# Optimization experiments

Hardware: AMD Instinct MI355X
Metric: run time of the kernel (lower is better)

Reference implementation:

```python
import jax, jax.numpy as jnp
import numpy as np

# --- config (matches init_kwargs) ---
D_MODEL = 512
N_HEADS = 8
DIM_HEAD = D_MODEL // N_HEADS  # 64
BUCKET_SIZE = 64
N_HASHES = 4
B = 4
N = 4096
SELF_ATTN_VALUE = -5e4  # TOKEN_SELF_ATTN_VALUE in reformer_pytorch


def setup_inputs() -> dict:
    key = jax.random.key(0)
    ks = jax.random.split(key, 8)
    n_buckets = N // BUCKET_SIZE
    dh = N_HEADS * DIM_HEAD
    return {
        "queries": jax.random.normal(ks[0], (B, N, D_MODEL), jnp.float32),
        "keys": jax.random.normal(ks[1], (B, N, D_MODEL), jnp.float32),      # unused by module
        "values": jax.random.normal(ks[2], (B, N, D_MODEL), jnp.float32),    # unused by module
        "W_qk": jax.random.normal(ks[3], (D_MODEL, dh), jnp.float32) / np.float32(np.sqrt(D_MODEL)),
        "W_v": jax.random.normal(ks[4], (D_MODEL, dh), jnp.float32) / np.float32(np.sqrt(D_MODEL)),
        "W_out": jax.random.normal(ks[5], (dh, D_MODEL), jnp.float32) / np.float32(np.sqrt(dh)),
        "b_out": jnp.zeros((D_MODEL,), jnp.float32),
        # random LSH rotations: generated fresh (non-learnable) in torch; fixed here for determinism
        "rotations": jax.random.normal(ks[6], (DIM_HEAD, N_HASHES, n_buckets // 2), jnp.float32),
    }


def _look_one_back(x):
    # concat each chunk with the previous chunk along the within-chunk axis
    return jnp.concatenate([x, jnp.roll(x, 1, axis=1)], axis=2)


def lsh_attention(qk, v, rotations):
    # qk, v: (BH, T, dh) shared-QK LSH attention (reformer_pytorch LSHAttention)
    bh, T, dh = qk.shape
    n_buckets = T // BUCKET_SIZE
    total = N_HASHES * T

    # --- hash_vectors: random rotations + argmax over [R, -R] ---
    rotated = jnp.einsum('btf,fhi->bhti', qk, rotations)          # (bh, n_hashes, T, nb/2)
    rotated = jnp.concatenate([rotated, -rotated], axis=-1)       # (bh, n_hashes, T, nb)
    buckets = jnp.argmax(rotated, axis=-1)                        # (bh, n_hashes, T)
    offsets = (jnp.arange(N_HASHES) * n_buckets)[None, :, None]
    buckets = (buckets + offsets).reshape(bh, total)

    # --- stable sort by (bucket, position); keys are unique ---
    ticker = jnp.broadcast_to(jnp.arange(total)[None, :], (bh, total))
    buckets_and_t = T * buckets + (ticker % T)
    sticker = jnp.argsort(buckets_and_t, axis=-1)                 # (bh, total)
    undo_sort = jnp.argsort(sticker, axis=-1)
    st = sticker % T                                              # original positions, sorted

    sqk = jnp.take_along_axis(qk, st[:, :, None], axis=1)         # (bh, total, dh)
    sv = jnp.take_along_axis(v, st[:, :, None], axis=1)

    # --- chunk into bins; attend within chunk + one chunk back ---
    chunks = N_HASHES * n_buckets                                 # per-chunk len == BUCKET_SIZE
    bq_t = st.reshape(bh, chunks, -1)
    bqk = sqk.reshape(bh, chunks, -1, dh)
    bv = sv.reshape(bh, chunks, -1, dh)

    bq = bqk
    bk = bqk / jnp.maximum(jnp.linalg.norm(bqk, axis=-1, keepdims=True), 1e-12)  # F.normalize

    bk = _look_one_back(bk)       # (bh, chunks, 2*bs, dh)
    bv = _look_one_back(bv)
    bkv_t = _look_one_back(bq_t)  # (bh, chunks, 2*bs)

    dots = jnp.einsum('bcie,bcje->bcij', bq, bk) * (dh ** -0.5)   # (bh, chunks, bs, 2*bs)
    self_mask = bq_t[:, :, :, None] == bkv_t[:, :, None, :]
    dots = jnp.where(self_mask, SELF_ATTN_VALUE, dots)

    lse = jax.scipy.special.logsumexp(dots, axis=-1, keepdims=True)
    probs = jnp.exp(dots - lse)
    bo = jnp.einsum('bcij,bcje->bcie', probs, bv)                 # (bh, chunks, bs, dh)

    so = bo.reshape(bh, total, dh)
    slogits = lse.reshape(bh, total)
    o = jnp.take_along_axis(so, undo_sort[:, :, None], axis=1)
    logits = jnp.take_along_axis(slogits, undo_sort, axis=1)

    o = o.reshape(bh, N_HASHES, T, dh)
    logits = logits.reshape(bh, N_HASHES, T, 1)
    # combine hash rounds by softmax over per-round logsumexps
    w = jnp.exp(logits - jax.scipy.special.logsumexp(logits, axis=1, keepdims=True))
    return jnp.sum(o * w, axis=1)                                 # (bh, T, dh)


def reference(queries, keys, values, W_qk, W_v, W_out, b_out, rotations):
    Bsz, T, _ = queries.shape
    qk = queries @ W_qk                                           # (B, T, H*dh), no bias
    v = queries @ W_v

    def merge(x):
        return x.reshape(Bsz, T, N_HEADS, DIM_HEAD).transpose(0, 2, 1, 3).reshape(Bsz * N_HEADS, T, DIM_HEAD)

    out = lsh_attention(merge(qk), merge(v), rotations)           # (B*H, T, dh)
    out = out.reshape(Bsz, N_HEADS, T, DIM_HEAD).transpose(0, 2, 1, 3).reshape(Bsz, T, N_HEADS * DIM_HEAD)
    return out @ W_out + b_out                                    # to_out (with bias)
```

## Files before the change

### kernel.cpp

```cpp
#include <hip/hip_runtime.h>

typedef unsigned int uint32;
typedef _Float16 f16;
typedef _Float16 f16x8 __attribute__((ext_vector_type(8)));
typedef float f32x4 __attribute__((ext_vector_type(4)));
typedef unsigned short u16x8 __attribute__((ext_vector_type(8)));

#define B_SZ 4
#define T_SZ 4096
#define DMODEL 512
#define NHEAD 8
#define DH 64
#define NHASH 4
#define BH (B_SZ*NHEAD)
#define NBUCK 256
#define TOT (NHASH*T_SZ)
#define M_TOK (B_SZ*T_SZ)

#define KSTRIDE 72
#define PSTRIDE 136

#define AMB_TAU 1.5e-3f

__global__ __launch_bounds__(256) void kprep(
    const float* __restrict__ Wqk, const float* __restrict__ Wv,
    const float* __restrict__ Wout, f16* __restrict__ Wth, f16* __restrict__ Wtl,
    const float* __restrict__ rot, f16* __restrict__ rotTh, f16* __restrict__ rotTl,
    const float* __restrict__ qin, f16* __restrict__ Ah, f16* __restrict__ Al,
    int* __restrict__ amb_cnt)
{
  int bx = blockIdx.x;
  int tid = threadIdx.x;
  if (bx == 0 && tid == 0) *amb_cnt = 0;
  if (bx < 6){
    int n = bx*256 + tid;
    int sel = n >> 9, col = n & 511;
    const float* src = (sel==0)? Wqk : (sel==1)? Wv : Wout;
    f16* dh = Wth + (size_t)n*512;
    f16* dl = Wtl + (size_t)n*512;
    for (int kb=0; kb<64; kb++){
      f16x8 hv, lv;
      #pragma unroll
      for (int e=0;e<8;e++){
        float v = src[(size_t)(kb*8+e)*512 + col];
        f16 h = (f16)v;
        hv[e] = h; lv[e] = (f16)(v - (float)h);
      }
      ((f16x8*)dh)[kb] = hv;
      ((f16x8*)dl)[kb] = lv;
    }
  } else if (bx == 6){
    if (tid < 128){
      int n = tid;
      f16* dh = rotTh + n*64;
      f16* dl = rotTl + n*64;
      for (int db=0; db<8; db++){
        f16x8 hv, lv;
        #pragma unroll
        for (int e=0;e<8;e++){
          float v = rot[(db*8+e)*128 + n];
          f16 h = (f16)v;
          hv[e] = h; lv[e] = (f16)(v - (float)h);
        }
        ((f16x8*)dh)[db] = hv;
        ((f16x8*)dl)[db] = lv;
      }
    }
  } else {
    size_t gid = (size_t)(bx - 7)*256 + tid;
    const float4* src = (const float4*)(qin) + gid*2;
    float4 x0 = src[0], x1 = src[1];
    float v[8] = {x0.x,x0.y,x0.z,x0.w, x1.x,x1.y,x1.z,x1.w};
    f16x8 h, l;
    #pragma unroll
    for (int e=0;e<8;e++){ f16 hh=(f16)v[e]; h[e]=hh; l[e]=(f16)(v[e]-(float)hh); }
    ((f16x8*)Ah)[gid] = h;
    ((f16x8*)Al)[gid] = l;
  }
}

__global__ __launch_bounds__(256) void g_qkv(const f16* __restrict__ Ah,
    const f16* __restrict__ Al, const f16* __restrict__ Wth, const f16* __restrict__ Wtl,
    f16* __restrict__ qk16, f16* __restrict__ qkl, f16* __restrict__ v16)
{
  __shared__ f16 ah[128*KSTRIDE], al[128*KSTRIDE], bh[128*KSTRIDE], bl[128*KSTRIDE];
  int tid = threadIdx.x;
  int m0 = blockIdx.x*128, n0 = blockIdx.y*128;
  int w = tid >> 6, lane = tid & 63;
  int wm = w >> 1, wn = w & 1;
  int c_lane = lane & 15, quad = lane >> 4;

  f32x4 acc[4][4];
  #pragma unroll
  for (int mi=0;mi<4;mi++)
    #pragma unroll
    for (int ni=0;ni<4;ni++) acc[mi][ni] = (f32x4){0.f,0.f,0.f,0.f};

  int sr = tid >> 1, sc = (tid & 1) * 32;

  f16x8 pA[4], pAl[4], pB[4], pBl[4];
  auto issue = [&](int kc){
    int k0 = kc*64;
    const f16x8* pah = (const f16x8*)(Ah + (size_t)(m0+sr)*512 + k0 + sc);
    const f16x8* pal = (const f16x8*)(Al + (size_t)(m0+sr)*512 + k0 + sc);
    const f16x8* pbh = (const f16x8*)(Wth + (size_t)(n0+sr)*512 + k0 + sc);
    const f16x8* pbl = (const f16x8*)(Wtl + (size_t)(n0+sr)*512 + k0 + sc);
    #pragma unroll
    for (int i=0;i<4;i++){ pA[i]=pah[i]; pAl[i]=pal[i]; pB[i]=pbh[i]; pBl[i]=pbl[i]; }
  };

  issue(0);

  for (int kc=0; kc<8; kc++){
    {
      f16x8* dah = (f16x8*)&ah[sr*KSTRIDE + sc];
      f16x8* dal = (f16x8*)&al[sr*KSTRIDE + sc];
      f16x8* dbh = (f16x8*)&bh[sr*KSTRIDE + sc];
      f16x8* dbl = (f16x8*)&bl[sr*KSTRIDE + sc];
      #pragma unroll
      for (int i=0;i<4;i++){ dah[i]=pA[i]; dal[i]=pAl[i]; dbh[i]=pB[i]; dbl[i]=pBl[i]; }
    }
    __syncthreads();
    if (kc < 7) issue(kc+1);
    f16x8 fah[4][2], fal[4][2], fbh[4][2], fbl[4][2];
    #pragma unroll
    for (int i=0;i<4;i++)
      #pragma unroll
      for (int kb=0;kb<2;kb++){
        int ma = (wm*64 + i*16 + c_lane)*KSTRIDE + kb*32 + quad*8;
        int nb = (wn*64 + i*16 + c_lane)*KSTRIDE + kb*32 + quad*8;
        fah[i][kb] = *(const f16x8*)&ah[ma];
        fal[i][kb] = *(const f16x8*)&al[ma];
        fbh[i][kb] = *(const f16x8*)&bh[nb];
        fbl[i][kb] = *(const f16x8*)&bl[nb];
      }
    #pragma unroll
    for (int kb=0;kb<2;kb++)
      #pragma unroll
      for (int p=0;p<3;p++)
        #pragma unroll
        for (int mi=0;mi<4;mi++)
          #pragma unroll
          for (int ni=0;ni<4;ni++){
            f16x8 a = (p==2)? fal[mi][kb] : fah[mi][kb];
            f16x8 b = (p==1)? fbl[ni][kb] : fbh[ni][kb];
            acc[mi][ni] = __builtin_amdgcn_mfma_f32_16x16x32_f16(a, b, acc[mi][ni], 0,0,0);
          }
    __syncthreads();
  }

  #pragma unroll
  for (int mi=0;mi<4;mi++)
    #pragma unroll
    for (int ni=0;ni<4;ni++)
      #pragma unroll
      for (int r=0;r<4;r++){
        int n = n0 + wn*64 + ni*16 + c_lane;
        int tok = m0 + wm*64 + mi*16 + quad*4 + r;
        float val = acc[mi][ni][r];
        int b = tok >> 12, tp = tok & 4095;
        if (n < 512){
          int head = n >> 6, dd = n & 63;
          size_t idx = ((size_t)(b*NHEAD+head)*T_SZ + tp)*DH + dd;
          f16 hv = (f16)val;
          qk16[idx] = hv;
          qkl[idx]  = (f16)(val - (float)hv);
        } else {
          int j = n - 512, head = j >> 6, dd = j & 63;
          size_t idx = ((size_t)(b*NHEAD+head)*T_SZ + tp)*DH + dd;
          v16[idx] = (f16)val;
        }
      }
}

__global__ __launch_bounds__(256) void g_out(const float* __restrict__ lse,
    const f16* __restrict__ o_f16, const f16* __restrict__ Wth, const f16* __restrict__ Wtl,
    const float* __restrict__ bout, float* __restrict__ out)
{
  __shared__ f16 ah[128*KSTRIDE], al[128*KSTRIDE], bh[128*KSTRIDE], bl[128*KSTRIDE];
  int tid = threadIdx.x;
  int m0 = blockIdx.x*128, n0 = blockIdx.y*128;
  int w = tid >> 6, lane = tid & 63;
  int wm = w >> 1, wn = w & 1;
  int c_lane = lane & 15, quad = lane >> 4;
  const f16* Bh_base = Wth + (size_t)1024*512;
  const f16* Bl_base = Wtl + (size_t)1024*512;

  f32x4 acc[4][4];
  #pragma unroll
  for (int mi=0;mi<4;mi++)
    #pragma unroll
    for (int ni=0;ni<4;ni++) acc[mi][ni] = (f32x4){0.f,0.f,0.f,0.f};

  int sr = tid >> 1, sc = (tid & 1) * 32;
  int tok = m0 + sr;
  int tb = tok >> 12, tt = tok & 4095;

  float pl0, pl1, pl2, pl3;
  f16x8 pr0[4], pr1[4], pr2[4], pr3[4];

  auto issueA = [&](int kc){
    size_t lbase = ((size_t)(tb*NHEAD + kc)*NHASH)*T_SZ + tt;
    pl0 = lse[lbase];
    pl1 = lse[lbase + T_SZ];
    pl2 = lse[lbase + 2*T_SZ];
    pl3 = lse[lbase + 3*T_SZ];
    const f16x8* r0 = (const f16x8*)(o_f16 + lbase*DH + sc);
    const f16x8* r1 = (const f16x8*)(o_f16 + (lbase + (size_t)T_SZ)*DH + sc);
    const f16x8* r2 = (const f16x8*)(o_f16 + (lbase + (size_t)2*T_SZ)*DH + sc);
    const f16x8* r3 = (const f16x8*)(o_f16 + (lbase + (size_t)3*T_SZ)*DH + sc);
    #pragma unroll
    for (int i=0;i<4;i++){ pr0[i]=r0[i]; pr1[i]=r1[i]; pr2[i]=r2[i]; pr3[i]=r3[i]; }
  };

  issueA(0);

  for (int kc=0; kc<8; kc++){
    int k0 = kc*64;
    {
      float M = fmaxf(fmaxf(pl0,pl1), fmaxf(pl2,pl3));
      float e0 = __expf(pl0-M), e1 = __expf(pl1-M), e2 = __expf(pl2-M), e3 = __expf(pl3-M);
      float inv = 1.0f/(e0+e1+e2+e3);
      float w0=e0*inv, w1=e1*inv, w2=e2*inv, w3=e3*inv;
      const f16x8* pbhp = (const f16x8*)(Bh_base + (size_t)(n0+sr)*512 + k0 + sc);
      const f16x8* pblp = (const f16x8*)(Bl_base + (size_t)(n0+sr)*512 + k0 + sc);
      f16x8* dah = (f16x8*)&ah[sr*KSTRIDE + sc];
      f16x8* dal = (f16x8*)&al[sr*KSTRIDE + sc];
      f16x8* dbh = (f16x8*)&bh[sr*KSTRIDE + sc];
      f16x8* dbl = (f16x8*)&bl[sr*KSTRIDE + sc];
      #pragma unroll
      for (int i=0;i<4;i++){
        f16x8 a = pr0[i], bb = pr1[i], cc = pr2[i], dd = pr3[i];
        f16x8 ho, lo;
        #pragma unroll
        for (int e=0;e<8;e++){
          float res = w0*(float)a[e] + w1*(float)bb[e] + w2*(float)cc[e] + w3*(float)dd[e];
          f16 hh = (f16)res;
          ho[e] = hh; lo[e] = (f16)(res - (float)hh);
        }
        dah[i] = ho; dal[i] = lo;
        dbh[i] = pbhp[i]; dbl[i] = pblp[i];
      }
    }
    __syncthreads();
    if (kc < 7) issueA(kc+1);
    f16x8 fah[4][2], fal[4][2], fbh[4][2], fbl[4][2];
    #pragma unroll
    for (int i=0;i<4;i++)
      #pragma unroll
      for (int kb=0;kb<2;kb++){
        int ma = (wm*64 + i*16 + c_lane)*KSTRIDE + kb*32 + quad*8;
        int nb = (wn*64 + i*16 + c_lane)*KSTRIDE + kb*32 + quad*8;
        fah[i][kb] = *(const f16x8*)&ah[ma];
        fal[i][kb] = *(const f16x8*)&al[ma];
        fbh[i][kb] = *(const f16x8*)&bh[nb];
        fbl[i][kb] = *(const f16x8*)&bl[nb];
      }
    #pragma unroll
    for (int kb=0;kb<2;kb++)
      #pragma unroll
      for (int p=0;p<3;p++)
        #pragma unroll
        for (int mi=0;mi<4;mi++)
          #pragma unroll
          for (int ni=0;ni<4;ni++){
            f16x8 a = (p==2)? fal[mi][kb] : fah[mi][kb];
            f16x8 b = (p==1)? fbl[ni][kb] : fbh[ni][kb];
            acc[mi][ni] = __builtin_amdgcn_mfma_f32_16x16x32_f16(a, b, acc[mi][ni], 0,0,0);
          }
    __syncthreads();
  }

  #pragma unroll
  for (int mi=0;mi<4;mi++)
    #pragma unroll
    for (int ni=0;ni<4;ni++){
      int n = n0 + wn*64 + ni*16 + c_lane;
      float bn = bout[n];
      #pragma unroll
      for (int r=0;r<4;r++){
        int tk2 = m0 + wm*64 + mi*16 + quad*4 + r;
        out[(size_t)tk2*512 + n] = acc[mi][ni][r] + bn;
      }
    }
}

__global__ __launch_bounds__(256, 4) void k2_mfma(const f16* __restrict__ qkh,
    const f16* __restrict__ qkl, const f16* __restrict__ rotTh, const f16* __restrict__ rotTl,
    unsigned short* __restrict__ bucket,
    int* __restrict__ amb_list, int* __restrict__ amb_cnt)
{
  int tid = threadIdx.x;
  int w = tid >> 6, lane = tid & 63;
  int c_lane = lane & 15, quad = lane >> 4;
  int tok0 = (blockIdx.x*4 + w)*16;
  size_t rowb = (size_t)(tok0 + c_lane)*64;

  f16x8 tbh[2], tbl[2];
  #pragma unroll
  for (int kb=0;kb<2;kb++){
    tbh[kb] = *(const f16x8*)&qkh[rowb + kb*32 + quad*8];
    tbl[kb] = *(const f16x8*)&qkl[rowb + kb*32 + quad*8];
  }

  f32x4 acc[8];
  #pragma unroll
  for (int mi=0;mi<8;mi++) acc[mi] = (f32x4){0.f,0.f,0.f,0.f};

  #pragma unroll
  for (int mi=0;mi<8;mi++){
    int aoff = (mi*16 + c_lane)*64;
    #pragma unroll
    for (int kb=0;kb<2;kb++){
      f16x8 arh = *(const f16x8*)&rotTh[aoff + kb*32 + quad*8];
      f16x8 arl = *(const f16x8*)&rotTl[aoff + kb*32 + quad*8];
      acc[mi] = __builtin_amdgcn_mfma_f32_16x16x32_f16(arh, tbh[kb], acc[mi], 0,0,0);
      acc[mi] = __builtin_amdgcn_mfma_f32_16x16x32_f16(arl, tbh[kb], acc[mi], 0,0,0);
      acc[mi] = __builtin_amdgcn_mfma_f32_16x16x32_f16(arh, tbl[kb], acc[mi], 0,0,0);
    }
  }

  int tokg = tok0 + c_lane;
  int bhh = tokg >> 12, t = tokg & 4095;

  #pragma unroll
  for (int h=0; h<4; h++){
    float m1 = -1e30f, m2 = -1e30f, ssq = 0.f; int b1 = 0;
    #pragma unroll
    for (int u=0; u<8; u++){
      float v = acc[2*h + (u>>2)][u&3];
      int bidd = (u>>2)*16 + quad*4 + (u&3);
      ssq += v*v;
      if (v > m1){ m2=m1; m1=v; b1=bidd; } else if (v > m2) m2=v;
      float nv = -v;
      if (nv > m1){ m2=m1; m1=nv; b1=bidd+32; } else if (nv > m2) m2=nv;
    }
    #pragma unroll
    for (int d2=16; d2<64; d2<<=1){
      float om1 = __shfl_xor(m1, d2);
      float om2 = __shfl_xor(m2, d2);
      int   ob1 = __shfl_xor(b1, d2);
      ssq += __shfl_xor(ssq, d2);
      if (om1 > m1){ m2 = fmaxf(m1, om2); m1 = om1; b1 = ob1; }
      else          { m2 = fmaxf(m2, om1); }
    }
    if (quad == 0){
      float rms = sqrtf(ssq * (1.0f/32.0f));
      if (m1 - m2 < AMB_TAU * rms){
        int idx = atomicAdd(amb_cnt, 1);
        amb_list[idx] = (bhh<<14) | (h<<12) | t;
      } else {
        bucket[((bhh*NHASH + h)<<12) + t] = (unsigned short)(b1 + (h<<6));
      }
    }
  }
}

__global__ __launch_bounds__(256) void k2_fix(const float* __restrict__ qin,
    const float* __restrict__ Wqk, const float* __restrict__ rot,
    const int* __restrict__ amb_list, const int* __restrict__ amb_cnt,
    unsigned short* __restrict__ bucket)
{
  __shared__ __align__(16) float qs[512];
  __shared__ double part[4][64];
  __shared__ double qk64[64];
  __shared__ double accs[32];
  int n = *amb_cnt;
  int tid = threadIdx.x;
  int j = tid & 63, chunk = tid >> 6;
  for (int it = blockIdx.x; it < n; it += gridDim.x){
    int gid = amb_list[it];
    int t = gid & (T_SZ-1);
    int h = (gid >> 12) & 3;
    int bh = gid >> 14;
    int b = bh >> 3, head = bh & 7;
    if (tid < 128)
      *(float4*)&qs[tid*4] = ((const float4*)(qin + ((size_t)b*T_SZ + t)*DMODEL))[tid];
    __syncthreads();
    const float* wcol = Wqk + head*64 + j;
    int d0 = chunk*128;
    double s = 0.0;
    #pragma unroll 16
    for (int d=0; d<128; d++)
      s += (double)qs[d0+d] * (double)wcol[(size_t)(d0+d)*512];
    part[chunk][j] = s;
    __syncthreads();
    if (tid < 64)
      qk64[tid] = ((part[0][tid] + part[1][tid]) + part[2][tid]) + part[3][tid];
    __syncthreads();
    if (tid < 32){
      double a = 0.0;
      #pragma unroll 16
      for (int f=0; f<64; f++)
        a += qk64[f] * (double)rot[f*(NHASH*32) + h*32 + tid];
      accs[tid] = a;
    }
    __syncthreads();
    if (tid == 0){
      double best = accs[0]; int bk = 0;
      for (int k=1;k<64;k++){
        double vv = (k<32)? accs[k] : -accs[k-32];
        if (vv > best){ best = vv; bk = k; }
      }
      bucket[((bh*NHASH + h)<<12) + t] = (unsigned short)(bk + (h<<6));
    }
    __syncthreads();
  }
}

__global__ __launch_bounds__(256) void k3_scan(const unsigned short* __restrict__ bucket,
    int* __restrict__ starts){
  __shared__ int s[256];
  int bh = blockIdx.x, tid = threadIdx.x;
  s[tid] = 0;
  __syncthreads();
  const u16x8* b8 = (const u16x8*)(bucket + ((size_t)bh*NHASH << 12));
  for (int i = tid; i < 2048; i += 256){
    u16x8 x = b8[i];
    #pragma unroll
    for (int e=0;e<8;e++) atomicAdd(&s[x[e]], 1);
  }
  __syncthreads();
  int v = s[tid];
  __syncthreads();
  for (int off=1; off<256; off<<=1){
    int a = (tid >= off) ? s[tid-off] : 0;
    __syncthreads();
    s[tid] += a;
    __syncthreads();
  }
  starts[bh*256 + tid] = s[tid] - v;
}

__global__ __launch_bounds__(64) void k3b_scatter(const unsigned short* __restrict__ bucket,
    const int* __restrict__ starts, int* __restrict__ st)
{
  int blk = blockIdx.x;
  int bh = blk >> 8; int g = blk & 255; int h = g >> 6;
  int lane = threadIdx.x;
  const u16x8* brow8 = (const u16x8*)(bucket + ((size_t)(bh*NHASH + h) << 12)) + lane*8;
  unsigned short gv = (unsigned short)g;
  u16x8 seg[8];
  int cnt = 0;
  #pragma unroll
  for (int i=0;i<8;i++){
    seg[i] = brow8[i];
    #pragma unroll
    for (int e=0;e<8;e++) cnt += (seg[i][e] == gv) ? 1 : 0;
  }
  int pre = cnt;
  #pragma unroll
  for (int d=1; d<64; d<<=1){
    int o = __shfl_up(pre, d);
    if (lane >= d) pre += o;
  }
  int base = starts[bh*NBUCK + g] + (pre - cnt);
  int t0 = lane*64;
  int* dst = st + bh*TOT;
  #pragma unroll
  for (int i=0;i<8;i++)
    #pragma unroll
    for (int e=0;e<8;e++)
      if (seg[i][e] == gv) dst[base++] = t0 + i*8 + e;
}

__global__ __launch_bounds__(256, 4) void k4_attn(const f16* __restrict__ qk16,
    const f16* __restrict__ v16, const int* __restrict__ st,
    float* __restrict__ lse_out, f16* __restrict__ o_out)
{
  __shared__ __align__(16) char smem[36864];
  f16*   k_lds   = (f16*)smem;
  f16*   p_lds   = (f16*)smem;
  f16*   vT      = (f16*)(smem + 18432);
  float* invnorm = (float*)(smem + 35840);
  int*   kv_t    = (int*)(smem + 36352);

  int bid = blockIdx.x;
  int swz = (bid & 7) * 1024 + (bid >> 3);
  int bh = swz >> 8; int c = swz & 255;
  int h = c >> 6; int cp = (c + 255) & 255;
  int tid = threadIdx.x;
  int w = tid >> 6, lane = tid & 63;
  int c_lane = lane & 15, quad = lane >> 4;
  const int* strow = st + bh*TOT;

  if (tid < 128){
    int row = tid;
    int slot = (row < 64) ? (c*64 + row) : (cp*64 + row - 64);
    int t = strow[slot];
    kv_t[row] = t;
    const f16x8* kr = (const f16x8*)(qk16 + ((size_t)bh*T_SZ + t)*DH);
    const f16x8* vr = (const f16x8*)(v16  + ((size_t)bh*T_SZ + t)*DH);
    f16x8 kv[8], vv[8];
    float ss = 0.f;
    #pragma unroll
    for (int i=0;i<8;i++){
      f16x8 x = kr[i]; kv[i] = x;
      vv[i] = vr[i];
      #pragma unroll
      for (int e=0;e<8;e++){ float f = (float)x[e]; ss += f*f; }
    }
    invnorm[row] = 1.0f / fmaxf(sqrtf(ss), 1e-12f);
    f16x8* kd = (f16x8*)&k_lds[row*KSTRIDE];
    #pragma unroll
    for (int i=0;i<8;i++) kd[i] = kv[i];
    #pragma unroll
    for (int i=0;i<8;i++){
      #pragma unroll
      for (int e=0;e<8;e++) vT[(i*8+e)*PSTRIDE + row] = vv[i][e];
    }
  }
  __syncthreads();

  int mi = w;
  f16x8 aq[2];
  #pragma unroll
  for (int kb=0;kb<2;kb++)
    aq[kb] = *(const f16x8*)&k_lds[(mi*16 + c_lane)*KSTRIDE + kb*32 + quad*8];

  f32x4 accS[8];
  #pragma unroll
  for (int ni=0;ni<8;ni++) accS[ni] = (f32x4){0.f,0.f,0.f,0.f};

  #pragma unroll
  for (int ni=0;ni<8;ni++){
    int rowb = ni*16 + c_lane;
    f16 sc = (f16)invnorm[rowb];
    f16x8 b0 = *(const f16x8*)&k_lds[rowb*KSTRIDE + 0*32 + quad*8];
    f16x8 b1 = *(const f16x8*)&k_lds[rowb*KSTRIDE + 1*32 + quad*8];
    b0 *= sc; b1 *= sc;
    accS[ni] = __builtin_amdgcn_mfma_f32_16x16x32_f16(aq[0], b0, accS[ni], 0,0,0);
    accS[ni] = __builtin_amdgcn_mfma_f32_16x16x32_f16(aq[1], b1, accS[ni], 0,0,0);
  }

  int tq[4];
  #pragma unroll
  for (int r=0;r<4;r++) tq[r] = kv_t[mi*16 + quad*4 + r];
  int tk[8];
  #pragma unroll
  for (int ni=0;ni<8;ni++) tk[ni] = kv_t[ni*16 + c_lane];

  float mrow[4], lrow[4];
  #pragma unroll
  for (int r=0;r<4;r++){
    float mx = -1e30f;
    #pragma unroll
    for (int ni=0;ni<8;ni++){
      float s = accS[ni][r] * 0.125f;
      if (tk[ni] == tq[r]) s = -50000.0f;
      accS[ni][r] = s;
      mx = fmaxf(mx, s);
    }
    mx = fmaxf(mx, __shfl_xor(mx, 1));
    mx = fmaxf(mx, __shfl_xor(mx, 2));
    mx = fmaxf(mx, __shfl_xor(mx, 4));
    mx = fmaxf(mx, __shfl_xor(mx, 8));
    mrow[r] = mx;
    float ls = 0.f;
    #pragma unroll
    for (int ni=0;ni<8;ni++){
      float e = __expf(accS[ni][r] - mx);
      accS[ni][r] = e;
      ls += e;
    }
    ls += __shfl_xor(ls, 1);
    ls += __shfl_xor(ls, 2);
    ls += __shfl_xor(ls, 4);
    ls += __shfl_xor(ls, 8);
    lrow[r] = ls;
  }

  __syncthreads();

  #pragma unroll
  for (int ni=0;ni<8;ni++)
    #pragma unroll
    for (int r=0;r<4;r++)
      p_lds[(mi*16 + quad*4 + r)*PSTRIDE + ni*16 + c_lane] = (f16)accS[ni][r];

  f16x8 pa[4];
  #pragma unroll
  for (int kb=0;kb<4;kb++)
    pa[kb] = *(const f16x8*)&p_lds[(mi*16 + c_lane)*PSTRIDE + kb*32 + quad*8];

  size_t rowbase = (size_t)(bh*NHASH + h)*T_SZ;
  #pragma unroll
  for (int ni2=0;ni2<4;ni2++){
    f16x8 bv[4];
    #pragma unroll
    for (int kb=0;kb<4;kb++)
      bv[kb] = *(const f16x8*)&vT[(ni2*16 + c_lane)*PSTRIDE + kb*32 + quad*8];
    f32x4 accO = (f32x4){0.f,0.f,0.f,0.f};
    #pragma unroll
    for (int kb=0;kb<4;kb++)
      accO = __builtin_amdgcn_mfma_f32_16x16x32_f16(pa[kb], bv[kb], accO, 0,0,0);
    #pragma unroll
    for (int r=0;r<4;r++){
      float invl = 1.0f / lrow[r];
      f16* orow = o_out + (rowbase + tq[r])*DH;
      orow[ni2*16 + c_lane] = (f16)(accO[r] * invl);
    }
  }
  #pragma unroll
  for (int r=0;r<4;r++){
    if (c_lane == 0)
      lse_out[rowbase + tq[r]] = mrow[r] + logf(lrow[r]);
  }
}

extern "C" void kernel_launch(void* const* d_in, const int* in_sizes, int n_in,
                              void* d_out, int out_size, void* d_ws, size_t ws_size,
                              hipStream_t stream) {
  const float* queries = (const float*)d_in[0];
  const float* Wqk     = (const float*)d_in[3];
  const float* Wv      = (const float*)d_in[4];
  const float* Wout    = (const float*)d_in[5];
  const float* bout    = (const float*)d_in[6];
  const float* rot     = (const float*)d_in[7];
  float* out = (float*)d_out;

  const size_t SZ_F16  = (size_t)BH*T_SZ*DH*2;
  const size_t SZ_WT   = (size_t)1536*512*2;
  const size_t SZ_ROT  = (size_t)128*64*2;
  const size_t SZ_O    = (size_t)BH*NHASH*T_SZ*DH*2;
  const size_t OFS_X      = 0;
  const size_t OFS_AH     = OFS_X    + 2*SZ_F16;
  const size_t OFS_AL     = OFS_AH   + SZ_F16;
  const size_t OFS_QK16   = OFS_AL   + SZ_F16;
  const size_t OFS_V16    = OFS_QK16 + SZ_F16;
  const size_t OFS_WTH    = OFS_V16  + SZ_F16;
  const size_t OFS_WTL    = OFS_WTH  + SZ_WT;
  const size_t OFS_ROTH   = OFS_WTL  + SZ_WT;
  const size_t OFS_ROTL   = OFS_ROTH + SZ_ROT;
  const size_t OFS_O      = OFS_ROTL + SZ_ROT;
  const size_t OFS_BUCKET = OFS_O    + SZ_O;
  const size_t OFS_HIST   = OFS_BUCKET + (size_t)BH*NHASH*T_SZ*2;
  const size_t OFS_STARTS = OFS_HIST   + (size_t)BH*NBUCK*4;
  const size_t OFS_ST     = OFS_STARTS + (size_t)BH*NBUCK*4;
  const size_t OFS_LSE    = OFS_ST     + (size_t)BH*TOT*4;
  const size_t OFS_AMB    = OFS_LSE    + (size_t)BH*NHASH*T_SZ*4;
  const size_t OFS_CNT    = OFS_AMB    + (size_t)BH*NHASH*T_SZ*4;
  const size_t WS_NEEDED  = OFS_CNT    + 256;
  if (ws_size < WS_NEEDED) return;

  char* ws = (char*)d_ws;
  f16*      qkl    = (f16*)(ws + OFS_X);
  f16*      Ah     = (f16*)(ws + OFS_AH);
  f16*      Al     = (f16*)(ws + OFS_AL);
  f16*      qk16   = (f16*)(ws + OFS_QK16);
  f16*      v16    = (f16*)(ws + OFS_V16);
  f16*      Wth    = (f16*)(ws + OFS_WTH);
  f16*      Wtl    = (f16*)(ws + OFS_WTL);
  f16*      rotTh  = (f16*)(ws + OFS_ROTH);
  f16*      rotTl  = (f16*)(ws + OFS_ROTL);
  f16*      o_f16  = (f16*)(ws + OFS_O);
  unsigned short* bucket = (unsigned short*)(ws + OFS_BUCKET);
  int*      starts = (int*)(ws + OFS_STARTS);
  int*      st     = (int*)(ws + OFS_ST);
  float*    lse    = (float*)(ws + OFS_LSE);
  int*      amb    = (int*)(ws + OFS_AMB);
  int*      cnt    = (int*)(ws + OFS_CNT);

  kprep     <<<7 + (M_TOK*DMODEL/8)/256, 256, 0, stream>>>(Wqk, Wv, Wout, Wth, Wtl,
                                       rot, rotTh, rotTl, queries, Ah, Al, cnt);
  g_qkv     <<<dim3(M_TOK/128, 8), 256, 0, stream>>>(Ah, Al, Wth, Wtl, qk16, qkl, v16);
  k2_mfma   <<<(BH*T_SZ)/64, 256, 0, stream>>>(qk16, qkl, rotTh, rotTl, bucket, amb, cnt);
  k2_fix    <<<2048, 256, 0, stream>>>(queries, Wqk, rot, amb, cnt, bucket);
  k3_scan   <<<BH, 256, 0, stream>>>(bucket, starts);
  k3b_scatter<<<BH*NBUCK, 64, 0, stream>>>(bucket, starts, st);
  k4_attn   <<<BH*256, 256, 0, stream>>>(qk16, v16, st, lse, o_f16);
  g_out     <<<dim3(M_TOK/128, 4), 256, 0, stream>>>(lse, o_f16, Wth, Wtl, bout, out);
}
```

Baseline: 476.8 us.

## Fuse query fp16 hi/lo split into QKV GEMM and coalesce bucket scatter

The fp32 query split into fp16 high/low parts moves from the prep kernel into the QKV GEMM's global-to-LDS staging, so the Ah/Al intermediate is no longer written and re-read. The weight-prep part of kprep is spread over 48 blocks instead of 6 to raise parallelism. The bucket scatter now uses coalesced per-step loads with ballot and popcount instead of contiguous per-lane segments plus a shuffle scan. The trade-off is more conversion work per GEMM tile, since each of the 8 column blocks redoes the split, and 64 serial loop steps in the scatter.

```diff
diff --git a/kernel.cpp b/kernel.cpp
--- a/kernel.cpp
+++ b/kernel.cpp
@@ -26,19 +26,19 @@
     const float* __restrict__ Wqk, const float* __restrict__ Wv,
     const float* __restrict__ Wout, f16* __restrict__ Wth, f16* __restrict__ Wtl,
     const float* __restrict__ rot, f16* __restrict__ rotTh, f16* __restrict__ rotTl,
-    const float* __restrict__ qin, f16* __restrict__ Ah, f16* __restrict__ Al,
     int* __restrict__ amb_cnt)
 {
   int bx = blockIdx.x;
   int tid = threadIdx.x;
   if (bx == 0 && tid == 0) *amb_cnt = 0;
-  if (bx < 6){
-    int n = bx*256 + tid;
+  if (bx < 48){
+    int rg = bx >> 3, kc = bx & 7;
+    int n = rg*256 + tid;
     int sel = n >> 9, col = n & 511;
     const float* src = (sel==0)? Wqk : (sel==1)? Wv : Wout;
     f16* dh = Wth + (size_t)n*512;
     f16* dl = Wtl + (size_t)n*512;
-    for (int kb=0; kb<64; kb++){
+    for (int kb=kc*8; kb<kc*8+8; kb++){
       f16x8 hv, lv;
       #pragma unroll
       for (int e=0;e<8;e++){
@@ -49,7 +49,7 @@
       ((f16x8*)dh)[kb] = hv;
       ((f16x8*)dl)[kb] = lv;
     }
-  } else if (bx == 6){
+  } else {
     if (tid < 128){
       int n = tid;
       f16* dh = rotTh + n*64;
@@ -66,21 +66,11 @@
         ((f16x8*)dl)[db] = lv;
       }
     }
-  } else {
-    size_t gid = (size_t)(bx - 7)*256 + tid;
-    const float4* src = (const float4*)(qin) + gid*2;
-    float4 x0 = src[0], x1 = src[1];
-    float v[8] = {x0.x,x0.y,x0.z,x0.w, x1.x,x1.y,x1.z,x1.w};
-    f16x8 h, l;
-    #pragma unroll
-    for (int e=0;e<8;e++){ f16 hh=(f16)v[e]; h[e]=hh; l[e]=(f16)(v[e]-(float)hh); }
-    ((f16x8*)Ah)[gid] = h;
-    ((f16x8*)Al)[gid] = l;
-  }
-}
-
-__global__ __launch_bounds__(256) void g_qkv(const f16* __restrict__ Ah,
-    const f16* __restrict__ Al, const f16* __restrict__ Wth, const f16* __restrict__ Wtl,
+  }
+}
+
+__global__ __launch_bounds__(256) void g_qkv(const float* __restrict__ qin,
+    const f16* __restrict__ Wth, const f16* __restrict__ Wtl,
     f16* __restrict__ qk16, f16* __restrict__ qkl, f16* __restrict__ v16)
 {
   __shared__ f16 ah[128*KSTRIDE], al[128*KSTRIDE], bh[128*KSTRIDE], bl[128*KSTRIDE];
@@ -98,15 +88,17 @@
 
   int sr = tid >> 1, sc = (tid & 1) * 32;
 
-  f16x8 pA[4], pAl[4], pB[4], pBl[4];
+  float4 pQ[8];
+  f16x8 pB[4], pBl[4];
   auto issue = [&](int kc){
     int k0 = kc*64;
-    const f16x8* pah = (const f16x8*)(Ah + (size_t)(m0+sr)*512 + k0 + sc);
-    const f16x8* pal = (const f16x8*)(Al + (size_t)(m0+sr)*512 + k0 + sc);
+    const float4* pq = (const float4*)(qin + (size_t)(m0+sr)*512 + k0 + sc);
     const f16x8* pbh = (const f16x8*)(Wth + (size_t)(n0+sr)*512 + k0 + sc);
     const f16x8* pbl = (const f16x8*)(Wtl + (size_t)(n0+sr)*512 + k0 + sc);
     #pragma unroll
-    for (int i=0;i<4;i++){ pA[i]=pah[i]; pAl[i]=pal[i]; pB[i]=pbh[i]; pBl[i]=pbl[i]; }
+    for (int i=0;i<8;i++) pQ[i] = pq[i];
+    #pragma unroll
+    for (int i=0;i<4;i++){ pB[i]=pbh[i]; pBl[i]=pbl[i]; }
   };
 
   issue(0);
@@ -118,7 +110,18 @@
       f16x8* dbh = (f16x8*)&bh[sr*KSTRIDE + sc];
       f16x8* dbl = (f16x8*)&bl[sr*KSTRIDE + sc];
       #pragma unroll
-      for (int i=0;i<4;i++){ dah[i]=pA[i]; dal[i]=pAl[i]; dbh[i]=pB[i]; dbl[i]=pBl[i]; }
+      for (int i=0;i<4;i++){
+        float v[8] = {pQ[2*i].x, pQ[2*i].y, pQ[2*i].z, pQ[2*i].w,
+                      pQ[2*i+1].x, pQ[2*i+1].y, pQ[2*i+1].z, pQ[2*i+1].w};
+        f16x8 ho, lo;
+        #pragma unroll
+        for (int e=0;e<8;e++){
+          f16 hh = (f16)v[e];
+          ho[e] = hh; lo[e] = (f16)(v[e] - (float)hh);
+        }
+        dah[i] = ho; dal[i] = lo;
+        dbh[i] = pB[i]; dbl[i] = pBl[i];
+      }
     }
     __syncthreads();
     if (kc < 7) issue(kc+1);
@@ -438,30 +441,18 @@
   int blk = blockIdx.x;
   int bh = blk >> 8; int g = blk & 255; int h = g >> 6;
   int lane = threadIdx.x;
-  const u16x8* brow8 = (const u16x8*)(bucket + ((size_t)(bh*NHASH + h) << 12)) + lane*8;
-  unsigned short gv = (unsigned short)g;
-  u16x8 seg[8];
-  int cnt = 0;
-  #pragma unroll
-  for (int i=0;i<8;i++){
-    seg[i] = brow8[i];
-    #pragma unroll
-    for (int e=0;e<8;e++) cnt += (seg[i][e] == gv) ? 1 : 0;
-  }
-  int pre = cnt;
-  #pragma unroll
-  for (int d=1; d<64; d<<=1){
-    int o = __shfl_up(pre, d);
-    if (lane >= d) pre += o;
-  }
-  int base = starts[bh*NBUCK + g] + (pre - cnt);
-  int t0 = lane*64;
-  int* dst = st + bh*TOT;
-  #pragma unroll
-  for (int i=0;i<8;i++)
-    #pragma unroll
-    for (int e=0;e<8;e++)
-      if (seg[i][e] == gv) dst[base++] = t0 + i*8 + e;
+  const unsigned short* brow = bucket + ((bh*NHASH + h)<<12);
+  int base = starts[bh*NBUCK + g];
+  for (int step=0; step<64; step++){
+    int t = step*64 + lane;
+    bool pred = (brow[t] == (unsigned short)g);
+    unsigned long long mask = __ballot(pred);
+    if (pred){
+      int off = __popcll(mask & ((1ull<<lane) - 1ull));
+      st[bh*TOT + base + off] = t;
+    }
+    base += __popcll(mask);
+  }
 }
 
 __global__ __launch_bounds__(256, 4) void k4_attn(const f16* __restrict__ qk16,
@@ -645,8 +636,6 @@
 
   char* ws = (char*)d_ws;
   f16*      qkl    = (f16*)(ws + OFS_X);
-  f16*      Ah     = (f16*)(ws + OFS_AH);
-  f16*      Al     = (f16*)(ws + OFS_AL);
   f16*      qk16   = (f16*)(ws + OFS_QK16);
   f16*      v16    = (f16*)(ws + OFS_V16);
   f16*      Wth    = (f16*)(ws + OFS_WTH);
@@ -661,9 +650,8 @@
   int*      amb    = (int*)(ws + OFS_AMB);
   int*      cnt    = (int*)(ws + OFS_CNT);
 
-  kprep     <<<7 + (M_TOK*DMODEL/8)/256, 256, 0, stream>>>(Wqk, Wv, Wout, Wth, Wtl,
-                                       rot, rotTh, rotTl, queries, Ah, Al, cnt);
-  g_qkv     <<<dim3(M_TOK/128, 8), 256, 0, stream>>>(Ah, Al, Wth, Wtl, qk16, qkl, v16);
+  kprep     <<<49, 256, 0, stream>>>(Wqk, Wv, Wout, Wth, Wtl, rot, rotTh, rotTl, cnt);
+  g_qkv     <<<dim3(M_TOK/128, 8), 256, 0, stream>>>(queries, Wth, Wtl, qk16, qkl, v16);
   k2_mfma   <<<(BH*T_SZ)/64, 256, 0, stream>>>(qk16, qkl, rotTh, rotTl, bucket, amb, cnt);
   k2_fix    <<<2048, 256, 0, stream>>>(queries, Wqk, rot, amb, cnt, bucket);
   k3_scan   <<<BH, 256, 0, stream>>>(bucket, starts);
```

Result: faster. 434.6 us (-8.9%).
